# Kernel optimization log

Hardware: AMD Instinct MI355X
Metric: run time of the kernel (lower is better)

## Reference

```python
import jax, jax.numpy as jnp
import numpy as np

VOCAB = 1000
MAX_T = 1000  # max_episode_length
L = 64        # instruction length


def _uniform(key, shape, fan_in, fan_out):
    bound = float(np.sqrt(6.0 / (fan_in + fan_out)))
    return jax.random.uniform(key, shape, jnp.float32, -bound, bound)


def setup_inputs() -> dict:
    key = jax.random.key(0)
    ks = jax.random.split(key, 20)
    s = float(1.0 / np.sqrt(256.0))
    inp = {}
    inp['x'] = jax.random.normal(ks[0], (1, 400), jnp.float32)
    inp['input_inst'] = jax.random.randint(ks[1], (1, L), 0, VOCAB)
    inp['tx'] = jax.random.randint(ks[2], (1,), 0, MAX_T + 1)
    inp['hx'] = jax.random.normal(ks[3], (1, 256), jnp.float32) * 0.1
    inp['cx'] = jax.random.normal(ks[4], (1, 256), jnp.float32) * 0.1
    inp['img1_w'] = _uniform(ks[5], (128, 400), 400, 128); inp['img1_b'] = jnp.zeros((128,), jnp.float32)
    inp['img2_w'] = _uniform(ks[6], (128, 128), 128, 128); inp['img2_b'] = jnp.zeros((128,), jnp.float32)
    inp['img3_w'] = _uniform(ks[7], (128, 128), 128, 128); inp['img3_b'] = jnp.zeros((128,), jnp.float32)
    inp['emb'] = jax.random.normal(ks[8], (VOCAB, 32), jnp.float32)
    inp['gru_wi'] = jax.random.uniform(ks[9], (768, 32), jnp.float32, -s, s)
    inp['gru_wh'] = jax.random.uniform(ks[10], (768, 256), jnp.float32, -s, s)
    inp['gru_bi'] = jnp.zeros((768,), jnp.float32); inp['gru_bh'] = jnp.zeros((768,), jnp.float32)
    inp['attn_w'] = _uniform(ks[11], (128, 256), 256, 128); inp['attn_b'] = jnp.zeros((128,), jnp.float32)
    inp['time_emb'] = jax.random.normal(ks[12], (MAX_T + 1, 32), jnp.float32)
    inp['lin_w'] = _uniform(ks[13], (256, 128), 128, 256); inp['lin_b'] = jnp.zeros((256,), jnp.float32)
    inp['lstm_wi'] = jax.random.uniform(ks[14], (1024, 256), jnp.float32, -s, s)
    inp['lstm_wh'] = jax.random.uniform(ks[15], (1024, 256), jnp.float32, -s, s)
    inp['lstm_bi'] = jnp.zeros((1024,), jnp.float32); inp['lstm_bh'] = jnp.zeros((1024,), jnp.float32)
    inp['crit_w'] = jax.random.normal(ks[16], (1, 288), jnp.float32) * 0.06
    inp['crit_b'] = jnp.zeros((1,), jnp.float32)
    inp['act_w'] = jax.random.normal(ks[17], (4, 288), jnp.float32) * 0.01
    inp['act_b'] = jnp.zeros((4,), jnp.float32)
    return inp


def _linear(x, w, b):
    return x @ w.T + b


def reference(x, input_inst, tx, hx, cx,
              img1_w, img1_b, img2_w, img2_b, img3_w, img3_b,
              emb, gru_wi, gru_wh, gru_bi, gru_bh,
              attn_w, attn_b, time_emb, lin_w, lin_b,
              lstm_wi, lstm_wh, lstm_bi, lstm_bh,
              crit_w, crit_b, act_w, act_b):
    # image MLP: 400 -> 128 -> 128 -> 128
    h = jax.nn.relu(_linear(x.reshape(x.shape[0], -1), img1_w, img1_b))
    h = jax.nn.relu(_linear(h, img2_w, img2_b))
    x_image_rep = jax.nn.relu(_linear(h, img3_w, img3_b))  # (1,128)

    # GRU encoder over instruction tokens (torch gate order: r, z, n)
    emb_seq = emb[input_inst[0]]  # (L, 32)

    def gru_step(hg, e):
        gi = gru_wi @ e + gru_bi        # (768,)
        gh = gru_wh @ hg + gru_bh       # (768,)
        ir, iz, i_n = jnp.split(gi, 3)
        hr, hz, hn = jnp.split(gh, 3)
        r = jax.nn.sigmoid(ir + hr)
        z = jax.nn.sigmoid(iz + hz)
        n = jnp.tanh(i_n + r * hn)
        return (1.0 - z) * n + z * hg, None

    h_enc, _ = jax.lax.scan(gru_step, jnp.zeros((256,), x.dtype), emb_seq)
    x_instr_rep = h_enc[None, :]  # (1,256)

    # gated attention fusion
    x_attention = jax.nn.sigmoid(_linear(x_instr_rep, attn_w, attn_b))  # (1,128)
    fused = x_image_rep * x_attention
    fused = jax.nn.relu(_linear(fused, lin_w, lin_b))  # (1,256)

    # LSTMCell (torch gate order: i, f, g, o)
    gates = fused @ lstm_wi.T + lstm_bi + hx @ lstm_wh.T + lstm_bh  # (1,1024)
    i_g, f_g, g_g, o_g = jnp.split(gates, 4, axis=1)
    c_new = jax.nn.sigmoid(f_g) * cx + jax.nn.sigmoid(i_g) * jnp.tanh(g_g)
    h_new = jax.nn.sigmoid(o_g) * jnp.tanh(c_new)

    t_emb = time_emb[tx].reshape(-1, 32)  # (1,32)
    feat = jnp.concatenate([h_new, t_emb], axis=1)  # (1,288)
    return _linear(feat, crit_w, crit_b), _linear(feat, act_w, act_b), h_new, c_new
```

## Files before the change

### kernel.cpp

```cpp
#include <hip/hip_runtime.h>
#include <math.h>


#define SENT_U 0xFFC0DEADu

#define WS_HBUF   0
#define WS_FLAGS  16640
#define WS_IMG    16704
#define WS_GATESH 16832
#define WS_FUSED  17856
#define WS_HNEW   18112

__device__ __forceinline__ float dot4(const float4 a, const float4 b){
  return a.x*b.x + a.y*b.y + a.z*b.z + a.w*b.w;
}
__device__ __forceinline__ float sigm(float x){ return 1.f/(1.f+expf(-x)); }
__device__ __forceinline__ float aload(const float* p){
  return __hip_atomic_load(p, __ATOMIC_RELAXED, __HIP_MEMORY_SCOPE_AGENT);
}
__device__ __forceinline__ void astore(float* p, float v){
  __hip_atomic_store(p, v, __ATOMIC_RELAXED, __HIP_MEMORY_SCOPE_AGENT);
}

__global__ __launch_bounds__(256) void a3c_init(float* __restrict__ ws){
  const int i = blockIdx.x*256 + threadIdx.x;
  ((unsigned*)(ws + WS_HBUF + 256))[i] = SENT_U;
  if (i < 2) ((int*)(ws + WS_FLAGS))[i] = 0;
}

__global__ __launch_bounds__(256) void a3c_main(
    const int*   __restrict__ inst, const float* __restrict__ emb,
    const float* __restrict__ gwi,  const float* __restrict__ gwh,
    const float* __restrict__ gbi,  const float* __restrict__ gbh,
    const float* __restrict__ x,
    const float* __restrict__ i1w,  const float* __restrict__ i1b,
    const float* __restrict__ i2w,  const float* __restrict__ i2b,
    const float* __restrict__ i3w,  const float* __restrict__ i3b,
    const float* __restrict__ hx,   const float* __restrict__ lwh,
    const float* __restrict__ lbh,  float* __restrict__ ws)
{
  const int b = blockIdx.x;
  const int t = threadIdx.x;

  if (b < 8) {
    __shared__ __align__(16) float h_lds[256];
    __shared__ float gi_lds[64*96];
    __shared__ __align__(16) float emb_lds[64*32];
    const int u   = t >> 3;
    const int sub = t & 7;
    const int U   = b*32 + u;

    float4 wv0[8], wv1[8], wv2[8];
    {
      const float4* p0 = (const float4*)(gwh + (0*256 + U)*256 + sub*32);
      const float4* p1 = (const float4*)(gwh + (1*256 + U)*256 + sub*32);
      const float4* p2 = (const float4*)(gwh + (2*256 + U)*256 + sub*32);
      #pragma unroll
      for (int k=0;k<8;++k){ wv0[k]=p0[k]; wv1[k]=p1[k]; wv2[k]=p2[k]; }
    }
    const float bh0 = gbh[U], bh1 = gbh[256+U], bh2 = gbh[512+U];

    for (int i=t; i<64*32; i+=256)
      emb_lds[i] = emb[inst[i>>5]*32 + (i&31)];
    h_lds[t] = 0.f;
    __syncthreads();

    if (t < 192){
      const int lr = t>>1, half = t&1;
      const int g = lr>>5, ul = lr&31;
      const int grow = (g<<8) + b*32 + ul;
      float4 wi[8];
      const float4* wip = (const float4*)(gwi + grow*32);
      #pragma unroll
      for (int k=0;k<8;++k) wi[k]=wip[k];
      const float bi = gbi[grow];
      for (int s=half*32; s<half*32+32; ++s){
        const float4* e4 = (const float4*)(emb_lds + s*32);
        float acc = bi;
        #pragma unroll
        for (int k=0;k<8;++k) acc += dot4(wi[k], e4[k]);
        gi_lds[s*96 + lr] = acc;
      }
    }
    __syncthreads();

    float* hb = ws + WS_HBUF;
    for (int s=0; s<64; ++s){
      const float4* h4 = (const float4*)(h_lds + sub*32);
      float p0=0.f, p1=0.f, p2=0.f;
      #pragma unroll
      for (int k=0;k<8;++k){
        const float4 h = h4[k];
        p0 += dot4(wv0[k], h);
        p1 += dot4(wv1[k], h);
        p2 += dot4(wv2[k], h);
      }
      #pragma unroll
      for (int off=4; off; off>>=1){
        p0 += __shfl_down(p0, off, 8);
        p1 += __shfl_down(p1, off, 8);
        p2 += __shfl_down(p2, off, 8);
      }
      const float h_old = h_lds[U];
      if (sub == 0){
        const float* gis = gi_lds + s*96;
        const float r = sigm(gis[u]      + p0 + bh0);
        const float z = sigm(gis[32 + u] + p1 + bh1);
        const float n = tanhf(gis[64 + u] + r*(p2 + bh2));
        astore(&hb[(s+1)*256 + U], (1.f - z)*n + z*h_old);
      }
      __syncthreads();
      float v;
      do { v = aload(&hb[(s+1)*256 + t]); } while (__float_as_uint(v) == SENT_U);
      h_lds[t] = v;
      __syncthreads();
    }

  } else if (b == 8) {
    __shared__ __align__(16) float x_lds[400];
    __shared__ __align__(16) float h1[128];
    __shared__ __align__(16) float h2[128];
    x_lds[t] = x[t];
    if (t < 144) x_lds[256+t] = x[256+t];
    __syncthreads();
    {
      const int o = t>>1, half = t&1;
      const float4* wr = (const float4*)(i1w + o*400 + half*200);
      const float4* xr = (const float4*)(x_lds + half*200);
      float acc = 0.f;
      #pragma unroll 5
      for (int k=0;k<50;++k) acc += dot4(wr[k], xr[k]);
      acc += __shfl_down(acc, 1, 2);
      if (half == 0) h1[o] = fmaxf(acc + i1b[o], 0.f);
    }
    __syncthreads();
    if (t < 128){
      const float4* wr = (const float4*)(i2w + t*128);
      const float4* h4 = (const float4*)h1;
      float acc = i2b[t];
      #pragma unroll 8
      for (int k=0;k<32;++k) acc += dot4(wr[k], h4[k]);
      h2[t] = fmaxf(acc, 0.f);
    }
    __syncthreads();
    if (t < 128){
      const float4* wr = (const float4*)(i3w + t*128);
      const float4* h4 = (const float4*)h2;
      float acc = i3b[t];
      #pragma unroll 8
      for (int k=0;k<32;++k) acc += dot4(wr[k], h4[k]);
      ws[WS_IMG + t] = fmaxf(acc, 0.f);
    }

  } else {
    __shared__ __align__(16) float hx_lds[256];
    hx_lds[t] = hx[t];
    __syncthreads();
    const int R = (b-9)*256 + t;
    const float4* wr = (const float4*)(lwh + R*256);
    const float4* h4 = (const float4*)hx_lds;
    float acc = lbh[R];
    #pragma unroll 8
    for (int k=0;k<64;++k) acc += dot4(wr[k], h4[k]);
    ws[WS_GATESH + R] = acc;
  }
}

__global__ __launch_bounds__(256) void a3c_tail(
    const float* __restrict__ aw,  const float* __restrict__ ab,
    const float* __restrict__ lw,  const float* __restrict__ lb,
    const float* __restrict__ lwi, const float* __restrict__ lbi,
    const float* __restrict__ cx,  const int*   __restrict__ tx,
    const float* __restrict__ temb,
    const float* __restrict__ cw,  const float* __restrict__ cb,
    const float* __restrict__ acw, const float* __restrict__ acb,
    float* __restrict__ ws, float* __restrict__ out)
{
  const int b = blockIdx.x;
  const int t = threadIdx.x;
  int* F = (int*)(ws + WS_FLAGS);

  if (b == 0) {
    __shared__ __align__(16) float henc[256];
    __shared__ __align__(16) float f0[128];
    __shared__ __align__(16) float feat[288];
    __shared__ float red[4];
    henc[t] = ws[WS_HBUF + 64*256 + t];
    __syncthreads();
    if (t < 128){
      const float4* wr = (const float4*)(aw + t*256);
      const float4* h4 = (const float4*)henc;
      float acc = ab[t];
      #pragma unroll 8
      for (int k=0;k<64;++k) acc += dot4(wr[k], h4[k]);
      f0[t] = ws[WS_IMG + t] * sigm(acc);
    }
    __syncthreads();
    {
      const float4* wr = (const float4*)(lw + t*128);
      const float4* h4 = (const float4*)f0;
      float acc = lb[t];
      #pragma unroll 8
      for (int k=0;k<32;++k) acc += dot4(wr[k], h4[k]);
      astore(ws + WS_FUSED + t, fmaxf(acc, 0.f));
    }
    __syncthreads();
    if (t == 0){
      __threadfence();
      __hip_atomic_store(&F[0], 1, __ATOMIC_RELEASE, __HIP_MEMORY_SCOPE_AGENT);
      while (__hip_atomic_load(&F[1], __ATOMIC_ACQUIRE, __HIP_MEMORY_SCOPE_AGENT) < 4){}
    }
    __syncthreads();
    feat[t] = aload(ws + WS_HNEW + t);
    if (t < 32) feat[256+t] = temb[tx[0]*32 + t];
    __syncthreads();
    for (int o=0; o<5; ++o){
      const float* wrow = (o==0) ? cw : (acw + (o-1)*288);
      float pr = feat[t]*wrow[t];
      if (t < 32) pr += feat[256+t]*wrow[256+t];
      #pragma unroll
      for (int off=32; off; off>>=1) pr += __shfl_down(pr, off, 64);
      if ((t&63)==0) red[t>>6] = pr;
      __syncthreads();
      if (t == 0) out[o] = red[0]+red[1]+red[2]+red[3] + (o==0 ? cb[0] : acb[o-1]);
      __syncthreads();
    }

  } else {
    const int p = b - 1;
    __shared__ __align__(16) float fused_lds[256];
    __shared__ float gv[256];
    const int g = t >> 6, ul = t & 63;
    const int R = (g<<8) + p*64 + ul;
    const float4* wr = (const float4*)(lwi + R*256);
    float pf = 0.f;
    for (int k=0;k<64;++k){ float4 w = wr[k]; pf += w.x+w.y+w.z+w.w; }
    asm volatile("" :: "v"(pf));
    const float gh = ws[WS_GATESH + R] + lbi[R];
    if (t == 0){
      while (__hip_atomic_load(&F[0], __ATOMIC_ACQUIRE, __HIP_MEMORY_SCOPE_AGENT) == 0){}
    }
    __syncthreads();
    fused_lds[t] = aload(ws + WS_FUSED + t);
    __syncthreads();
    float acc = gh;
    const float4* f4 = (const float4*)fused_lds;
    #pragma unroll 8
    for (int k=0;k<64;++k) acc += dot4(wr[k], f4[k]);
    gv[t] = acc;
    __syncthreads();
    if (t < 64){
      const int u2 = p*64 + t;
      const float iv = gv[t], fv = gv[64+t], gg = gv[128+t], ov = gv[192+t];
      const float c = sigm(fv)*cx[u2] + sigm(iv)*tanhf(gg);
      const float h = sigm(ov)*tanhf(c);
      out[5   + u2] = h;
      out[261 + u2] = c;
      astore(ws + WS_HNEW + u2, h);
    }
    __syncthreads();
    if (t == 0){
      __threadfence();
      __hip_atomic_fetch_add(&F[1], 1, __ATOMIC_RELEASE, __HIP_MEMORY_SCOPE_AGENT);
    }
  }
}

extern "C" void kernel_launch(void* const* d_in, const int* in_sizes, int n_in,
                              void* d_out, int out_size, void* d_ws, size_t ws_size,
                              hipStream_t stream) {
  (void)in_sizes; (void)n_in; (void)out_size; (void)ws_size;
  const float* x    = (const float*)d_in[0];
  const int*   inst = (const int*)  d_in[1];
  const int*   tx   = (const int*)  d_in[2];
  const float* hx   = (const float*)d_in[3];
  const float* cx   = (const float*)d_in[4];
  const float* i1w  = (const float*)d_in[5];
  const float* i1b  = (const float*)d_in[6];
  const float* i2w  = (const float*)d_in[7];
  const float* i2b  = (const float*)d_in[8];
  const float* i3w  = (const float*)d_in[9];
  const float* i3b  = (const float*)d_in[10];
  const float* emb  = (const float*)d_in[11];
  const float* gwi  = (const float*)d_in[12];
  const float* gwh  = (const float*)d_in[13];
  const float* gbi  = (const float*)d_in[14];
  const float* gbh  = (const float*)d_in[15];
  const float* aw   = (const float*)d_in[16];
  const float* ab   = (const float*)d_in[17];
  const float* temb = (const float*)d_in[18];
  const float* lw   = (const float*)d_in[19];
  const float* lb   = (const float*)d_in[20];
  const float* lwi  = (const float*)d_in[21];
  const float* lwh  = (const float*)d_in[22];
  const float* lbi  = (const float*)d_in[23];
  const float* lbh  = (const float*)d_in[24];
  const float* cw   = (const float*)d_in[25];
  const float* cb   = (const float*)d_in[26];
  const float* acw  = (const float*)d_in[27];
  const float* acb  = (const float*)d_in[28];
  float* ws  = (float*)d_ws;
  float* out = (float*)d_out;

  a3c_init<<<64, 256, 0, stream>>>(ws);
  a3c_main<<<13, 256, 0, stream>>>(inst, emb, gwi, gwh, gbi, gbh,
                                   x, i1w, i1b, i2w, i2b, i3w, i3b,
                                   hx, lwh, lbh, ws);
  a3c_tail<<<5, 256, 0, stream>>>(aw, ab, lw, lb, lwi, lbi, cx, tx, temb,
                                  cw, cb, acw, acb, ws, out);
}
```

Baseline: 151.2 us.

## Run GRU scan in one 768-thread block with fp16 register-resident weights

Replaces the 8-block GRU recurrence, which synchronised through global-memory sentinel polling, with a single 768-thread workgroup. Each thread keeps one full row of the hidden-weight matrix as packed fp16 in registers and uses fdot2, so each step needs only LDS and __syncthreads. Kernels are reordered into pre/scan/post and the flag spin-waits are dropped. Output heads are now summed with atomicAdd. The costs are reduced fp16 precision, heavy register pressure (128 packed regs per thread) and one workgroup doing all the serial work.

New measurement: 174.4 us. 15.4% more time.

```diff
diff --git a/kernel.cpp b/kernel.cpp
--- a/kernel.cpp
+++ b/kernel.cpp
@@ -2,124 +2,36 @@
 #include <math.h>
 
 
-#define SENT_U 0xFFC0DEADu
-
-#define WS_HBUF   0
-#define WS_FLAGS  16640
-#define WS_IMG    16704
-#define WS_GATESH 16832
-#define WS_FUSED  17856
-#define WS_HNEW   18112
+typedef __fp16 h2 __attribute__((ext_vector_type(2)));
+
+#define WS_IMG    0
+#define WS_GATESH 128
+#define WS_FUSED  1152
 
 __device__ __forceinline__ float dot4(const float4 a, const float4 b){
   return a.x*b.x + a.y*b.y + a.z*b.z + a.w*b.w;
 }
 __device__ __forceinline__ float sigm(float x){ return 1.f/(1.f+expf(-x)); }
-__device__ __forceinline__ float aload(const float* p){
-  return __hip_atomic_load(p, __ATOMIC_RELAXED, __HIP_MEMORY_SCOPE_AGENT);
-}
-__device__ __forceinline__ void astore(float* p, float v){
-  __hip_atomic_store(p, v, __ATOMIC_RELAXED, __HIP_MEMORY_SCOPE_AGENT);
-}
-
-__global__ __launch_bounds__(256) void a3c_init(float* __restrict__ ws){
-  const int i = blockIdx.x*256 + threadIdx.x;
-  ((unsigned*)(ws + WS_HBUF + 256))[i] = SENT_U;
-  if (i < 2) ((int*)(ws + WS_FLAGS))[i] = 0;
-}
-
-__global__ __launch_bounds__(256) void a3c_main(
-    const int*   __restrict__ inst, const float* __restrict__ emb,
-    const float* __restrict__ gwi,  const float* __restrict__ gwh,
-    const float* __restrict__ gbi,  const float* __restrict__ gbh,
+
+__global__ __launch_bounds__(256) void a3c_pre(
     const float* __restrict__ x,
-    const float* __restrict__ i1w,  const float* __restrict__ i1b,
-    const float* __restrict__ i2w,  const float* __restrict__ i2b,
-    const float* __restrict__ i3w,  const float* __restrict__ i3b,
-    const float* __restrict__ hx,   const float* __restrict__ lwh,
-    const float* __restrict__ lbh,  float* __restrict__ ws)
+    const float* __restrict__ i1w, const float* __restrict__ i1b,
+    const float* __restrict__ i2w, const float* __restrict__ i2b,
+    const float* __restrict__ i3w, const float* __restrict__ i3b,
+    const float* __restrict__ hx,  const float* __restrict__ lwh,
+    const float* __restrict__ lbh,
+    const int*   __restrict__ tx,  const float* __restrict__ temb,
+    const float* __restrict__ cw,  const float* __restrict__ cb,
+    const float* __restrict__ acw, const float* __restrict__ acb,
+    float* __restrict__ ws, float* __restrict__ out)
 {
   const int b = blockIdx.x;
   const int t = threadIdx.x;
 
-  if (b < 8) {
-    __shared__ __align__(16) float h_lds[256];
-    __shared__ float gi_lds[64*96];
-    __shared__ __align__(16) float emb_lds[64*32];
-    const int u   = t >> 3;
-    const int sub = t & 7;
-    const int U   = b*32 + u;
-
-    float4 wv0[8], wv1[8], wv2[8];
-    {
-      const float4* p0 = (const float4*)(gwh + (0*256 + U)*256 + sub*32);
-      const float4* p1 = (const float4*)(gwh + (1*256 + U)*256 + sub*32);
-      const float4* p2 = (const float4*)(gwh + (2*256 + U)*256 + sub*32);
-      #pragma unroll
-      for (int k=0;k<8;++k){ wv0[k]=p0[k]; wv1[k]=p1[k]; wv2[k]=p2[k]; }
-    }
-    const float bh0 = gbh[U], bh1 = gbh[256+U], bh2 = gbh[512+U];
-
-    for (int i=t; i<64*32; i+=256)
-      emb_lds[i] = emb[inst[i>>5]*32 + (i&31)];
-    h_lds[t] = 0.f;
-    __syncthreads();
-
-    if (t < 192){
-      const int lr = t>>1, half = t&1;
-      const int g = lr>>5, ul = lr&31;
-      const int grow = (g<<8) + b*32 + ul;
-      float4 wi[8];
-      const float4* wip = (const float4*)(gwi + grow*32);
-      #pragma unroll
-      for (int k=0;k<8;++k) wi[k]=wip[k];
-      const float bi = gbi[grow];
-      for (int s=half*32; s<half*32+32; ++s){
-        const float4* e4 = (const float4*)(emb_lds + s*32);
-        float acc = bi;
-        #pragma unroll
-        for (int k=0;k<8;++k) acc += dot4(wi[k], e4[k]);
-        gi_lds[s*96 + lr] = acc;
-      }
-    }
-    __syncthreads();
-
-    float* hb = ws + WS_HBUF;
-    for (int s=0; s<64; ++s){
-      const float4* h4 = (const float4*)(h_lds + sub*32);
-      float p0=0.f, p1=0.f, p2=0.f;
-      #pragma unroll
-      for (int k=0;k<8;++k){
-        const float4 h = h4[k];
-        p0 += dot4(wv0[k], h);
-        p1 += dot4(wv1[k], h);
-        p2 += dot4(wv2[k], h);
-      }
-      #pragma unroll
-      for (int off=4; off; off>>=1){
-        p0 += __shfl_down(p0, off, 8);
-        p1 += __shfl_down(p1, off, 8);
-        p2 += __shfl_down(p2, off, 8);
-      }
-      const float h_old = h_lds[U];
-      if (sub == 0){
-        const float* gis = gi_lds + s*96;
-        const float r = sigm(gis[u]      + p0 + bh0);
-        const float z = sigm(gis[32 + u] + p1 + bh1);
-        const float n = tanhf(gis[64 + u] + r*(p2 + bh2));
-        astore(&hb[(s+1)*256 + U], (1.f - z)*n + z*h_old);
-      }
-      __syncthreads();
-      float v;
-      do { v = aload(&hb[(s+1)*256 + t]); } while (__float_as_uint(v) == SENT_U);
-      h_lds[t] = v;
-      __syncthreads();
-    }
-
-  } else if (b == 8) {
+  if (b == 0) {
     __shared__ __align__(16) float x_lds[400];
     __shared__ __align__(16) float h1[128];
-    __shared__ __align__(16) float h2[128];
+    __shared__ __align__(16) float h2s[128];
     x_lds[t] = x[t];
     if (t < 144) x_lds[256+t] = x[256+t];
     __syncthreads();
@@ -140,23 +52,37 @@
       float acc = i2b[t];
       #pragma unroll 8
       for (int k=0;k<32;++k) acc += dot4(wr[k], h4[k]);
-      h2[t] = fmaxf(acc, 0.f);
+      h2s[t] = fmaxf(acc, 0.f);
     }
     __syncthreads();
     if (t < 128){
       const float4* wr = (const float4*)(i3w + t*128);
-      const float4* h4 = (const float4*)h2;
+      const float4* h4 = (const float4*)h2s;
       float acc = i3b[t];
       #pragma unroll 8
       for (int k=0;k<32;++k) acc += dot4(wr[k], h4[k]);
       ws[WS_IMG + t] = fmaxf(acc, 0.f);
     }
 
+  } else if (b == 5) {
+    if (t < 64){
+      float tv = 0.f;
+      if (t < 32) tv = temb[tx[0]*32 + t];
+      #pragma unroll
+      for (int o=0;o<5;++o){
+        const float* wrow = (o==0) ? cw : (acw + (o-1)*288);
+        float pr = (t < 32) ? tv*wrow[256+t] : 0.f;
+        #pragma unroll
+        for (int off=16; off; off>>=1) pr += __shfl_down(pr, off, 32);
+        if (t == 0) out[o] = pr + ((o==0) ? cb[0] : acb[o-1]);
+      }
+    }
+
   } else {
     __shared__ __align__(16) float hx_lds[256];
     hx_lds[t] = hx[t];
     __syncthreads();
-    const int R = (b-9)*256 + t;
+    const int R = (b-1)*256 + t;
     const float4* wr = (const float4*)(lwh + R*256);
     const float4* h4 = (const float4*)hx_lds;
     float acc = lbh[R];
@@ -166,102 +92,147 @@
   }
 }
 
-__global__ __launch_bounds__(256) void a3c_tail(
-    const float* __restrict__ aw,  const float* __restrict__ ab,
-    const float* __restrict__ lw,  const float* __restrict__ lb,
+__global__ __launch_bounds__(768) void a3c_scan(
+    const int*   __restrict__ inst, const float* __restrict__ emb,
+    const float* __restrict__ gwi,  const float* __restrict__ gwh,
+    const float* __restrict__ gbi,  const float* __restrict__ gbh,
+    const float* __restrict__ aw,   const float* __restrict__ ab,
+    const float* __restrict__ lw,   const float* __restrict__ lb,
+    float* __restrict__ ws)
+{
+  const int t = threadIdx.x;
+  __shared__ __fp16 gi16[64*768];
+  __shared__ __align__(16) h2 e16[1024];
+  __shared__ __align__(16) float h32[256];
+  __shared__ __align__(16) h2 h16[128];
+  __shared__ float pre[768];
+  __shared__ float hn[256];
+  __shared__ __align__(16) float f0[128];
+
+  for (int i=t; i<2048; i+=768)
+    ((__fp16*)e16)[i] = (__fp16)emb[inst[i>>5]*32 + (i&31)];
+  const float bh_t = gbh[t];
+  const float bi_t = gbi[t];
+  __syncthreads();
+
+  {
+    h2 wi[16];
+    const float4* wp = (const float4*)(gwi + t*32);
+    #pragma unroll
+    for (int k=0;k<8;++k){
+      float4 w = wp[k];
+      wi[2*k]   = __builtin_amdgcn_cvt_pkrtz(w.x, w.y);
+      wi[2*k+1] = __builtin_amdgcn_cvt_pkrtz(w.z, w.w);
+    }
+    for (int s=0;s<64;++s){
+      const h2* ep = e16 + s*16;
+      float a0 = bi_t, a1 = 0.f;
+      #pragma unroll
+      for (int k=0;k<8;++k)  a0 = __builtin_amdgcn_fdot2(wi[k], ep[k], a0, false);
+      #pragma unroll
+      for (int k=8;k<16;++k) a1 = __builtin_amdgcn_fdot2(wi[k], ep[k], a1, false);
+      gi16[s*768 + t] = (__fp16)(a0 + a1);
+    }
+  }
+
+  h2 wh[128];
+  {
+    const float4* wp = (const float4*)(gwh + t*256);
+    #pragma unroll
+    for (int k=0;k<64;++k){
+      float4 w = wp[k];
+      wh[2*k]   = __builtin_amdgcn_cvt_pkrtz(w.x, w.y);
+      wh[2*k+1] = __builtin_amdgcn_cvt_pkrtz(w.z, w.w);
+    }
+  }
+  if (t < 256){ h32[t] = 0.f; ((__fp16*)h16)[t] = (__fp16)0.f; }
+  __syncthreads();
+
+  for (int s=0;s<64;++s){
+    const float gi_s = (float)gi16[s*768 + t];
+    float a0 = bh_t, a1 = 0.f, a2 = 0.f, a3 = 0.f;
+    #pragma unroll
+    for (int k=0;  k<32; ++k) a0 = __builtin_amdgcn_fdot2(wh[k], h16[k], a0, false);
+    #pragma unroll
+    for (int k=32; k<64; ++k) a1 = __builtin_amdgcn_fdot2(wh[k], h16[k], a1, false);
+    #pragma unroll
+    for (int k=64; k<96; ++k) a2 = __builtin_amdgcn_fdot2(wh[k], h16[k], a2, false);
+    #pragma unroll
+    for (int k=96; k<128;++k) a3 = __builtin_amdgcn_fdot2(wh[k], h16[k], a3, false);
+    const float acc = (a0+a1)+(a2+a3);
+    if (t < 512) pre[t] = gi_s + acc;
+    else       { pre[t] = gi_s; hn[t-512] = acc; }
+    __syncthreads();
+    if (t < 256){
+      const float r  = sigm(pre[t]);
+      const float z  = sigm(pre[256+t]);
+      const float n  = tanhf(pre[512+t] + r*hn[t]);
+      const float hv = (1.f - z)*n + z*h32[t];
+      h32[t] = hv;
+      ((__fp16*)h16)[t] = (__fp16)hv;
+    }
+    __syncthreads();
+  }
+
+  if (t < 128){
+    const float4* wr = (const float4*)(aw + t*256);
+    const float4* h4 = (const float4*)h32;
+    float acc = ab[t];
+    #pragma unroll 8
+    for (int k=0;k<64;++k) acc += dot4(wr[k], h4[k]);
+    f0[t] = ws[WS_IMG + t] * sigm(acc);
+  }
+  __syncthreads();
+  if (t < 256){
+    const float4* wr = (const float4*)(lw + t*128);
+    const float4* h4 = (const float4*)f0;
+    float acc = lb[t];
+    #pragma unroll 8
+    for (int k=0;k<32;++k) acc += dot4(wr[k], h4[k]);
+    ws[WS_FUSED + t] = fmaxf(acc, 0.f);
+  }
+}
+
+__global__ __launch_bounds__(256) void a3c_post(
     const float* __restrict__ lwi, const float* __restrict__ lbi,
-    const float* __restrict__ cx,  const int*   __restrict__ tx,
-    const float* __restrict__ temb,
-    const float* __restrict__ cw,  const float* __restrict__ cb,
-    const float* __restrict__ acw, const float* __restrict__ acb,
+    const float* __restrict__ cx,
+    const float* __restrict__ cw,  const float* __restrict__ acw,
     float* __restrict__ ws, float* __restrict__ out)
 {
-  const int b = blockIdx.x;
+  const int p = blockIdx.x;
   const int t = threadIdx.x;
-  int* F = (int*)(ws + WS_FLAGS);
-
-  if (b == 0) {
-    __shared__ __align__(16) float henc[256];
-    __shared__ __align__(16) float f0[128];
-    __shared__ __align__(16) float feat[288];
-    __shared__ float red[4];
-    henc[t] = ws[WS_HBUF + 64*256 + t];
-    __syncthreads();
-    if (t < 128){
-      const float4* wr = (const float4*)(aw + t*256);
-      const float4* h4 = (const float4*)henc;
-      float acc = ab[t];
-      #pragma unroll 8
-      for (int k=0;k<64;++k) acc += dot4(wr[k], h4[k]);
-      f0[t] = ws[WS_IMG + t] * sigm(acc);
-    }
-    __syncthreads();
-    {
-      const float4* wr = (const float4*)(lw + t*128);
-      const float4* h4 = (const float4*)f0;
-      float acc = lb[t];
-      #pragma unroll 8
-      for (int k=0;k<32;++k) acc += dot4(wr[k], h4[k]);
-      astore(ws + WS_FUSED + t, fmaxf(acc, 0.f));
-    }
-    __syncthreads();
-    if (t == 0){
-      __threadfence();
-      __hip_atomic_store(&F[0], 1, __ATOMIC_RELEASE, __HIP_MEMORY_SCOPE_AGENT);
-      while (__hip_atomic_load(&F[1], __ATOMIC_ACQUIRE, __HIP_MEMORY_SCOPE_AGENT) < 4){}
-    }
-    __syncthreads();
-    feat[t] = aload(ws + WS_HNEW + t);
-    if (t < 32) feat[256+t] = temb[tx[0]*32 + t];
-    __syncthreads();
-    for (int o=0; o<5; ++o){
+  __shared__ __align__(16) float fused_lds[256];
+  __shared__ float gv[256];
+  __shared__ float hh[64];
+  fused_lds[t] = ws[WS_FUSED + t];
+  __syncthreads();
+  const int g = t>>6, ul = t&63;
+  const int R = (g<<8) + p*64 + ul;
+  const float4* wr = (const float4*)(lwi + R*256);
+  const float4* f4 = (const float4*)fused_lds;
+  float acc = ws[WS_GATESH + R] + lbi[R];
+  #pragma unroll 8
+  for (int k=0;k<64;++k) acc += dot4(wr[k], f4[k]);
+  gv[t] = acc;
+  __syncthreads();
+  if (t < 64){
+    const int u2 = p*64 + t;
+    const float iv = gv[t], fv = gv[64+t], gg = gv[128+t], ov = gv[192+t];
+    const float c = sigm(fv)*cx[u2] + sigm(iv)*tanhf(gg);
+    const float h = sigm(ov)*tanhf(c);
+    out[5   + u2] = h;
+    out[261 + u2] = c;
+    hh[t] = h;
+  }
+  __syncthreads();
+  if (t < 64){
+    #pragma unroll
+    for (int o=0;o<5;++o){
       const float* wrow = (o==0) ? cw : (acw + (o-1)*288);
-      float pr = feat[t]*wrow[t];
-      if (t < 32) pr += feat[256+t]*wrow[256+t];
+      float pr = hh[t]*wrow[p*64 + t];
       #pragma unroll
       for (int off=32; off; off>>=1) pr += __shfl_down(pr, off, 64);
-      if ((t&63)==0) red[t>>6] = pr;
-      __syncthreads();
-      if (t == 0) out[o] = red[0]+red[1]+red[2]+red[3] + (o==0 ? cb[0] : acb[o-1]);
-      __syncthreads();
-    }
-
-  } else {
-    const int p = b - 1;
-    __shared__ __align__(16) float fused_lds[256];
-    __shared__ float gv[256];
-    const int g = t >> 6, ul = t & 63;
-    const int R = (g<<8) + p*64 + ul;
-    const float4* wr = (const float4*)(lwi + R*256);
-    float pf = 0.f;
-    for (int k=0;k<64;++k){ float4 w = wr[k]; pf += w.x+w.y+w.z+w.w; }
-    asm volatile("" :: "v"(pf));
-    const float gh = ws[WS_GATESH + R] + lbi[R];
-    if (t == 0){
-      while (__hip_atomic_load(&F[0], __ATOMIC_ACQUIRE, __HIP_MEMORY_SCOPE_AGENT) == 0){}
-    }
-    __syncthreads();
-    fused_lds[t] = aload(ws + WS_FUSED + t);
-    __syncthreads();
-    float acc = gh;
-    const float4* f4 = (const float4*)fused_lds;
-    #pragma unroll 8
-    for (int k=0;k<64;++k) acc += dot4(wr[k], f4[k]);
-    gv[t] = acc;
-    __syncthreads();
-    if (t < 64){
-      const int u2 = p*64 + t;
-      const float iv = gv[t], fv = gv[64+t], gg = gv[128+t], ov = gv[192+t];
-      const float c = sigm(fv)*cx[u2] + sigm(iv)*tanhf(gg);
-      const float h = sigm(ov)*tanhf(c);
-      out[5   + u2] = h;
-      out[261 + u2] = c;
-      astore(ws + WS_HNEW + u2, h);
-    }
-    __syncthreads();
-    if (t == 0){
-      __threadfence();
-      __hip_atomic_fetch_add(&F[1], 1, __ATOMIC_RELEASE, __HIP_MEMORY_SCOPE_AGENT);
+      if (t == 0) atomicAdd(out + o, pr);
     }
   }
 }
@@ -302,10 +273,10 @@
   float* ws  = (float*)d_ws;
   float* out = (float*)d_out;
 
-  a3c_init<<<64, 256, 0, stream>>>(ws);
-  a3c_main<<<13, 256, 0, stream>>>(inst, emb, gwi, gwh, gbi, gbh,
-                                   x, i1w, i1b, i2w, i2b, i3w, i3b,
-                                   hx, lwh, lbh, ws);
-  a3c_tail<<<5, 256, 0, stream>>>(aw, ab, lw, lb, lwi, lbi, cx, tx, temb,
-                                  cw, cb, acw, acb, ws, out);
-}
+  a3c_pre <<<6, 256, 0, stream>>>(x, i1w, i1b, i2w, i2b, i3w, i3b,
+                                  hx, lwh, lbh, tx, temb, cw, cb, acw, acb,
+                                  ws, out);
+  a3c_scan<<<1, 768, 0, stream>>>(inst, emb, gwi, gwh, gbi, gbh,
+                                  aw, ab, lw, lb, ws);
+  a3c_post<<<4, 256, 0, stream>>>(lwi, lbi, cx, cw, acw, ws, out);
+}
```

## Co-locate GRU scan blocks on one XCD and restructure tail into post kernel

Applied to the files above, without the earlier changes.

Launches 120 candidate blocks and reads the XCC id from a hardware register, so that the first XCD to gather eight arrivals supplies the eight GRU-scan blocks. The 64-step per-step spin exchange then stays within one L2 and avoids cross-die coherence latency. The attention and fusion stage moves into scan block 0, which spin-waits on a sentinel-initialised image buffer. The LSTM and output heads move into a separate 4-block kernel that accumulates head outputs with atomicAdd, replacing the inter-block flag handshake. This adds launch overhead from surplus blocks and relies on the undocumented register layout and on co-residency for progress.

Result: faster. 147.6 us (-2.4%).

```diff
diff --git a/kernel.cpp b/kernel.cpp
--- a/kernel.cpp
+++ b/kernel.cpp
@@ -5,11 +5,12 @@
 #define SENT_U 0xFFC0DEADu
 
 #define WS_HBUF   0
-#define WS_FLAGS  16640
-#define WS_IMG    16704
-#define WS_GATESH 16832
-#define WS_FUSED  17856
-#define WS_HNEW   18112
+#define WS_CNT    16640
+#define WS_DESIG  16656
+#define WS_WTK    16657
+#define WS_IMG    16660
+#define WS_GATESH 16788
+#define WS_FUSED  17812
 
 __device__ __forceinline__ float dot4(const float4 a, const float4 b){
   return a.x*b.x + a.y*b.y + a.z*b.z + a.w*b.w;
@@ -23,177 +24,216 @@
 }
 
 __global__ __launch_bounds__(256) void a3c_init(float* __restrict__ ws){
-  const int i = blockIdx.x*256 + threadIdx.x;
-  ((unsigned*)(ws + WS_HBUF + 256))[i] = SENT_U;
-  if (i < 2) ((int*)(ws + WS_FLAGS))[i] = 0;
-}
-
-__global__ __launch_bounds__(256) void a3c_main(
+  const int b = blockIdx.x, t = threadIdx.x;
+  if (b < 64){
+    ((unsigned*)(ws + WS_HBUF + 256))[b*256 + t] = SENT_U;
+  } else {
+    if (t < 128)               ((unsigned*)(ws + WS_IMG))[t] = SENT_U;
+    else if (t < 144)          ((int*)(ws + WS_CNT))[t-128] = 0;
+    else if (t == 144)         ((int*)(ws + WS_DESIG))[0] = -1;
+    else if (t == 145)         ((int*)(ws + WS_WTK))[0] = 0;
+  }
+}
+
+__global__ __launch_bounds__(256) void a3c_scan(
     const int*   __restrict__ inst, const float* __restrict__ emb,
     const float* __restrict__ gwi,  const float* __restrict__ gwh,
     const float* __restrict__ gbi,  const float* __restrict__ gbh,
+    const float* __restrict__ aw,   const float* __restrict__ ab,
+    const float* __restrict__ lw,   const float* __restrict__ lb,
     const float* __restrict__ x,
     const float* __restrict__ i1w,  const float* __restrict__ i1b,
     const float* __restrict__ i2w,  const float* __restrict__ i2b,
     const float* __restrict__ i3w,  const float* __restrict__ i3b,
     const float* __restrict__ hx,   const float* __restrict__ lwh,
-    const float* __restrict__ lbh,  float* __restrict__ ws)
-{
-  const int b = blockIdx.x;
-  const int t = threadIdx.x;
-
-  if (b < 8) {
-    __shared__ __align__(16) float h_lds[256];
-    __shared__ float gi_lds[64*96];
-    __shared__ __align__(16) float emb_lds[64*32];
-    const int u   = t >> 3;
-    const int sub = t & 7;
-    const int U   = b*32 + u;
-
-    float4 wv0[8], wv1[8], wv2[8];
-    {
-      const float4* p0 = (const float4*)(gwh + (0*256 + U)*256 + sub*32);
-      const float4* p1 = (const float4*)(gwh + (1*256 + U)*256 + sub*32);
-      const float4* p2 = (const float4*)(gwh + (2*256 + U)*256 + sub*32);
-      #pragma unroll
-      for (int k=0;k<8;++k){ wv0[k]=p0[k]; wv1[k]=p1[k]; wv2[k]=p2[k]; }
-    }
-    const float bh0 = gbh[U], bh1 = gbh[256+U], bh2 = gbh[512+U];
-
-    for (int i=t; i<64*32; i+=256)
-      emb_lds[i] = emb[inst[i>>5]*32 + (i&31)];
-    h_lds[t] = 0.f;
-    __syncthreads();
-
-    if (t < 192){
-      const int lr = t>>1, half = t&1;
-      const int g = lr>>5, ul = lr&31;
-      const int grow = (g<<8) + b*32 + ul;
-      float4 wi[8];
-      const float4* wip = (const float4*)(gwi + grow*32);
-      #pragma unroll
-      for (int k=0;k<8;++k) wi[k]=wip[k];
-      const float bi = gbi[grow];
-      for (int s=half*32; s<half*32+32; ++s){
-        const float4* e4 = (const float4*)(emb_lds + s*32);
-        float acc = bi;
-        #pragma unroll
-        for (int k=0;k<8;++k) acc += dot4(wi[k], e4[k]);
-        gi_lds[s*96 + lr] = acc;
-      }
-    }
-    __syncthreads();
-
-    float* hb = ws + WS_HBUF;
-    for (int s=0; s<64; ++s){
-      const float4* h4 = (const float4*)(h_lds + sub*32);
-      float p0=0.f, p1=0.f, p2=0.f;
-      #pragma unroll
-      for (int k=0;k<8;++k){
-        const float4 h = h4[k];
-        p0 += dot4(wv0[k], h);
-        p1 += dot4(wv1[k], h);
-        p2 += dot4(wv2[k], h);
-      }
-      #pragma unroll
-      for (int off=4; off; off>>=1){
-        p0 += __shfl_down(p0, off, 8);
-        p1 += __shfl_down(p1, off, 8);
-        p2 += __shfl_down(p2, off, 8);
-      }
-      const float h_old = h_lds[U];
-      if (sub == 0){
-        const float* gis = gi_lds + s*96;
-        const float r = sigm(gis[u]      + p0 + bh0);
-        const float z = sigm(gis[32 + u] + p1 + bh1);
-        const float n = tanhf(gis[64 + u] + r*(p2 + bh2));
-        astore(&hb[(s+1)*256 + U], (1.f - z)*n + z*h_old);
-      }
-      __syncthreads();
-      float v;
-      do { v = aload(&hb[(s+1)*256 + t]); } while (__float_as_uint(v) == SENT_U);
-      h_lds[t] = v;
-      __syncthreads();
-    }
-
-  } else if (b == 8) {
-    __shared__ __align__(16) float x_lds[400];
-    __shared__ __align__(16) float h1[128];
-    __shared__ __align__(16) float h2[128];
-    x_lds[t] = x[t];
-    if (t < 144) x_lds[256+t] = x[256+t];
-    __syncthreads();
-    {
-      const int o = t>>1, half = t&1;
-      const float4* wr = (const float4*)(i1w + o*400 + half*200);
-      const float4* xr = (const float4*)(x_lds + half*200);
-      float acc = 0.f;
-      #pragma unroll 5
-      for (int k=0;k<50;++k) acc += dot4(wr[k], xr[k]);
-      acc += __shfl_down(acc, 1, 2);
-      if (half == 0) h1[o] = fmaxf(acc + i1b[o], 0.f);
-    }
-    __syncthreads();
-    if (t < 128){
-      const float4* wr = (const float4*)(i2w + t*128);
-      const float4* h4 = (const float4*)h1;
-      float acc = i2b[t];
-      #pragma unroll 8
-      for (int k=0;k<32;++k) acc += dot4(wr[k], h4[k]);
-      h2[t] = fmaxf(acc, 0.f);
-    }
-    __syncthreads();
-    if (t < 128){
-      const float4* wr = (const float4*)(i3w + t*128);
-      const float4* h4 = (const float4*)h2;
-      float acc = i3b[t];
-      #pragma unroll 8
-      for (int k=0;k<32;++k) acc += dot4(wr[k], h4[k]);
-      ws[WS_IMG + t] = fmaxf(acc, 0.f);
-    }
-
-  } else {
-    __shared__ __align__(16) float hx_lds[256];
-    hx_lds[t] = hx[t];
-    __syncthreads();
-    const int R = (b-9)*256 + t;
-    const float4* wr = (const float4*)(lwh + R*256);
-    const float4* h4 = (const float4*)hx_lds;
-    float acc = lbh[R];
-    #pragma unroll 8
-    for (int k=0;k<64;++k) acc += dot4(wr[k], h4[k]);
-    ws[WS_GATESH + R] = acc;
-  }
-}
-
-__global__ __launch_bounds__(256) void a3c_tail(
-    const float* __restrict__ aw,  const float* __restrict__ ab,
-    const float* __restrict__ lw,  const float* __restrict__ lb,
-    const float* __restrict__ lwi, const float* __restrict__ lbi,
-    const float* __restrict__ cx,  const int*   __restrict__ tx,
-    const float* __restrict__ temb,
-    const float* __restrict__ cw,  const float* __restrict__ cb,
-    const float* __restrict__ acw, const float* __restrict__ acb,
+    const float* __restrict__ lbh,
+    const int*   __restrict__ tx,   const float* __restrict__ temb,
+    const float* __restrict__ cw,   const float* __restrict__ cb,
+    const float* __restrict__ acw,  const float* __restrict__ acb,
     float* __restrict__ ws, float* __restrict__ out)
 {
   const int b = blockIdx.x;
   const int t = threadIdx.x;
-  int* F = (int*)(ws + WS_FLAGS);
-
-  if (b == 0) {
-    __shared__ __align__(16) float henc[256];
-    __shared__ __align__(16) float f0[128];
-    __shared__ __align__(16) float feat[288];
-    __shared__ float red[4];
-    henc[t] = ws[WS_HBUF + 64*256 + t];
+
+  if (b >= 120){
+    if (b == 120){
+      __shared__ __align__(16) float x_lds[400];
+      __shared__ __align__(16) float h1[128];
+      __shared__ __align__(16) float h2s[128];
+      x_lds[t] = x[t];
+      if (t < 144) x_lds[256+t] = x[256+t];
+      __syncthreads();
+      {
+        const int o = t>>1, half = t&1;
+        const float4* wr = (const float4*)(i1w + o*400 + half*200);
+        const float4* xr = (const float4*)(x_lds + half*200);
+        float acc = 0.f;
+        #pragma unroll 5
+        for (int k=0;k<50;++k) acc += dot4(wr[k], xr[k]);
+        acc += __shfl_down(acc, 1, 2);
+        if (half == 0) h1[o] = fmaxf(acc + i1b[o], 0.f);
+      }
+      __syncthreads();
+      if (t < 128){
+        const float4* wr = (const float4*)(i2w + t*128);
+        const float4* h4 = (const float4*)h1;
+        float acc = i2b[t];
+        #pragma unroll 8
+        for (int k=0;k<32;++k) acc += dot4(wr[k], h4[k]);
+        h2s[t] = fmaxf(acc, 0.f);
+      }
+      __syncthreads();
+      if (t < 128){
+        const float4* wr = (const float4*)(i3w + t*128);
+        const float4* h4 = (const float4*)h2s;
+        float acc = i3b[t];
+        #pragma unroll 8
+        for (int k=0;k<32;++k) acc += dot4(wr[k], h4[k]);
+        astore(ws + WS_IMG + t, fmaxf(acc, 0.f));
+      }
+    } else if (b == 125){
+      if (t < 64){
+        float tv = 0.f;
+        if (t < 32) tv = temb[tx[0]*32 + t];
+        #pragma unroll
+        for (int o=0;o<5;++o){
+          const float* wrow = (o==0) ? cw : (acw + (o-1)*288);
+          float pr = (t < 32) ? tv*wrow[256+t] : 0.f;
+          #pragma unroll
+          for (int off=16; off; off>>=1) pr += __shfl_down(pr, off, 32);
+          if (t == 0) out[o] = pr + ((o==0) ? cb[0] : acb[o-1]);
+        }
+      }
+    } else {
+      __shared__ __align__(16) float hx_lds[256];
+      hx_lds[t] = hx[t];
+      __syncthreads();
+      const int R = (b-121)*256 + t;
+      const float4* wr = (const float4*)(lwh + R*256);
+      const float4* h4 = (const float4*)hx_lds;
+      float acc = lbh[R];
+      #pragma unroll 8
+      for (int k=0;k<64;++k) acc += dot4(wr[k], h4[k]);
+      ws[WS_GATESH + R] = acc;
+    }
+    return;
+  }
+
+  __shared__ int s_role;
+  if (t == 0){
+    unsigned xcc;
+    asm volatile("s_getreg_b32 %0, hwreg(20, 0, 4)" : "=s"(xcc));
+    xcc &= 7u;
+    int* cnt   = (int*)(ws + WS_CNT);
+    int* desig = (int*)(ws + WS_DESIG);
+    int* wtk   = (int*)(ws + WS_WTK);
+    const int arr = __hip_atomic_fetch_add(&cnt[xcc], 1, __ATOMIC_RELAXED,
+                                           __HIP_MEMORY_SCOPE_AGENT);
+    if (arr == 7){
+      int exp = -1;
+      __hip_atomic_compare_exchange_strong(desig, &exp, (int)xcc,
+          __ATOMIC_RELEASE, __ATOMIC_RELAXED, __HIP_MEMORY_SCOPE_AGENT);
+    }
+    int d;
+    while ((d = __hip_atomic_load(desig, __ATOMIC_ACQUIRE,
+                                  __HIP_MEMORY_SCOPE_AGENT)) < 0)
+      __builtin_amdgcn_s_sleep(2);
+    int role = -1;
+    if ((int)xcc == d){
+      const int tk = __hip_atomic_fetch_add(wtk, 1, __ATOMIC_RELAXED,
+                                            __HIP_MEMORY_SCOPE_AGENT);
+      if (tk < 8) role = tk;
+    }
+    s_role = role;
+  }
+  __syncthreads();
+  const int r = s_role;
+  if (r < 0) return;
+
+  __shared__ __align__(16) float h_lds[256];
+  __shared__ float gi_lds[64*96];
+  __shared__ __align__(16) float emb_lds[64*32];
+  __shared__ __align__(16) float f0[128];
+  const int u   = t >> 3;
+  const int sub = t & 7;
+  const int U   = r*32 + u;
+
+  float4 wv0[8], wv1[8], wv2[8];
+  {
+    const float4* p0 = (const float4*)(gwh + (0*256 + U)*256 + sub*32);
+    const float4* p1 = (const float4*)(gwh + (1*256 + U)*256 + sub*32);
+    const float4* p2 = (const float4*)(gwh + (2*256 + U)*256 + sub*32);
+    #pragma unroll
+    for (int k=0;k<8;++k){ wv0[k]=p0[k]; wv1[k]=p1[k]; wv2[k]=p2[k]; }
+  }
+  const float bh0 = gbh[U], bh1 = gbh[256+U], bh2 = gbh[512+U];
+
+  for (int i=t; i<64*32; i+=256)
+    emb_lds[i] = emb[inst[i>>5]*32 + (i&31)];
+  h_lds[t] = 0.f;
+  __syncthreads();
+
+  if (t < 192){
+    const int lr = t>>1, half = t&1;
+    const int g = lr>>5, ul = lr&31;
+    const int grow = (g<<8) + r*32 + ul;
+    float4 wi[8];
+    const float4* wip = (const float4*)(gwi + grow*32);
+    #pragma unroll
+    for (int k=0;k<8;++k) wi[k]=wip[k];
+    const float bi = gbi[grow];
+    for (int s=half*32; s<half*32+32; ++s){
+      const float4* e4 = (const float4*)(emb_lds + s*32);
+      float acc = bi;
+      #pragma unroll
+      for (int k=0;k<8;++k) acc += dot4(wi[k], e4[k]);
+      gi_lds[s*96 + lr] = acc;
+    }
+  }
+  __syncthreads();
+
+  float* hb = ws + WS_HBUF;
+  for (int s=0; s<64; ++s){
+    const float4* h4 = (const float4*)(h_lds + sub*32);
+    float p0=0.f, p1=0.f, p2=0.f;
+    #pragma unroll
+    for (int k=0;k<8;++k){
+      const float4 h = h4[k];
+      p0 += dot4(wv0[k], h);
+      p1 += dot4(wv1[k], h);
+      p2 += dot4(wv2[k], h);
+    }
+    #pragma unroll
+    for (int off=4; off; off>>=1){
+      p0 += __shfl_down(p0, off, 8);
+      p1 += __shfl_down(p1, off, 8);
+      p2 += __shfl_down(p2, off, 8);
+    }
+    const float h_old = h_lds[U];
+    if (sub == 0){
+      const float* gis = gi_lds + s*96;
+      const float rr = sigm(gis[u]      + p0 + bh0);
+      const float zz = sigm(gis[32 + u] + p1 + bh1);
+      const float nn = tanhf(gis[64 + u] + rr*(p2 + bh2));
+      astore(&hb[(s+1)*256 + U], (1.f - zz)*nn + zz*h_old);
+    }
     __syncthreads();
+    float v;
+    do { v = aload(&hb[(s+1)*256 + t]); } while (__float_as_uint(v) == SENT_U);
+    h_lds[t] = v;
+    __syncthreads();
+  }
+
+  if (r == 0){
+    float im = 0.f;
     if (t < 128){
+      do { im = aload(ws + WS_IMG + t); } while (__float_as_uint(im) == SENT_U);
       const float4* wr = (const float4*)(aw + t*256);
-      const float4* h4 = (const float4*)henc;
+      const float4* h4 = (const float4*)h_lds;
       float acc = ab[t];
       #pragma unroll 8
       for (int k=0;k<64;++k) acc += dot4(wr[k], h4[k]);
-      f0[t] = ws[WS_IMG + t] * sigm(acc);
+      f0[t] = im * sigm(acc);
     }
     __syncthreads();
     {
@@ -202,66 +242,51 @@
       float acc = lb[t];
       #pragma unroll 8
       for (int k=0;k<32;++k) acc += dot4(wr[k], h4[k]);
-      astore(ws + WS_FUSED + t, fmaxf(acc, 0.f));
-    }
-    __syncthreads();
-    if (t == 0){
-      __threadfence();
-      __hip_atomic_store(&F[0], 1, __ATOMIC_RELEASE, __HIP_MEMORY_SCOPE_AGENT);
-      while (__hip_atomic_load(&F[1], __ATOMIC_ACQUIRE, __HIP_MEMORY_SCOPE_AGENT) < 4){}
-    }
-    __syncthreads();
-    feat[t] = aload(ws + WS_HNEW + t);
-    if (t < 32) feat[256+t] = temb[tx[0]*32 + t];
-    __syncthreads();
-    for (int o=0; o<5; ++o){
+      ws[WS_FUSED + t] = fmaxf(acc, 0.f);
+    }
+  }
+}
+
+__global__ __launch_bounds__(256) void a3c_post(
+    const float* __restrict__ lwi, const float* __restrict__ lbi,
+    const float* __restrict__ cx,
+    const float* __restrict__ cw,  const float* __restrict__ acw,
+    float* __restrict__ ws, float* __restrict__ out)
+{
+  const int p = blockIdx.x;
+  const int t = threadIdx.x;
+  __shared__ __align__(16) float fused_lds[256];
+  __shared__ float gv[256];
+  __shared__ float hh[64];
+  fused_lds[t] = ws[WS_FUSED + t];
+  __syncthreads();
+  const int g = t>>6, ul = t&63;
+  const int R = (g<<8) + p*64 + ul;
+  const float4* wr = (const float4*)(lwi + R*256);
+  const float4* f4 = (const float4*)fused_lds;
+  float acc = ws[WS_GATESH + R] + lbi[R];
+  #pragma unroll 8
+  for (int k=0;k<64;++k) acc += dot4(wr[k], f4[k]);
+  gv[t] = acc;
+  __syncthreads();
+  if (t < 64){
+    const int u2 = p*64 + t;
+    const float iv = gv[t], fv = gv[64+t], gg = gv[128+t], ov = gv[192+t];
+    const float c = sigm(fv)*cx[u2] + sigm(iv)*tanhf(gg);
+    const float h = sigm(ov)*tanhf(c);
+    out[5   + u2] = h;
+    out[261 + u2] = c;
+    hh[t] = h;
+  }
+  __syncthreads();
+  if (t < 64){
+    #pragma unroll
+    for (int o=0;o<5;++o){
       const float* wrow = (o==0) ? cw : (acw + (o-1)*288);
-      float pr = feat[t]*wrow[t];
-      if (t < 32) pr += feat[256+t]*wrow[256+t];
+      float pr = hh[t]*wrow[p*64 + t];
       #pragma unroll
       for (int off=32; off; off>>=1) pr += __shfl_down(pr, off, 64);
-      if ((t&63)==0) red[t>>6] = pr;
-      __syncthreads();
-      if (t == 0) out[o] = red[0]+red[1]+red[2]+red[3] + (o==0 ? cb[0] : acb[o-1]);
-      __syncthreads();
-    }
-
-  } else {
-    const int p = b - 1;
-    __shared__ __align__(16) float fused_lds[256];
-    __shared__ float gv[256];
-    const int g = t >> 6, ul = t & 63;
-    const int R = (g<<8) + p*64 + ul;
-    const float4* wr = (const float4*)(lwi + R*256);
-    float pf = 0.f;
-    for (int k=0;k<64;++k){ float4 w = wr[k]; pf += w.x+w.y+w.z+w.w; }
-    asm volatile("" :: "v"(pf));
-    const float gh = ws[WS_GATESH + R] + lbi[R];
-    if (t == 0){
-      while (__hip_atomic_load(&F[0], __ATOMIC_ACQUIRE, __HIP_MEMORY_SCOPE_AGENT) == 0){}
-    }
-    __syncthreads();
-    fused_lds[t] = aload(ws + WS_FUSED + t);
-    __syncthreads();
-    float acc = gh;
-    const float4* f4 = (const float4*)fused_lds;
-    #pragma unroll 8
-    for (int k=0;k<64;++k) acc += dot4(wr[k], f4[k]);
-    gv[t] = acc;
-    __syncthreads();
-    if (t < 64){
-      const int u2 = p*64 + t;
-      const float iv = gv[t], fv = gv[64+t], gg = gv[128+t], ov = gv[192+t];
-      const float c = sigm(fv)*cx[u2] + sigm(iv)*tanhf(gg);
-      const float h = sigm(ov)*tanhf(c);
-      out[5   + u2] = h;
-      out[261 + u2] = c;
-      astore(ws + WS_HNEW + u2, h);
-    }
-    __syncthreads();
-    if (t == 0){
-      __threadfence();
-      __hip_atomic_fetch_add(&F[1], 1, __ATOMIC_RELEASE, __HIP_MEMORY_SCOPE_AGENT);
+      if (t == 0) atomicAdd(out + o, pr);
     }
   }
 }
@@ -302,10 +327,11 @@
   float* ws  = (float*)d_ws;
   float* out = (float*)d_out;
 
-  a3c_init<<<64, 256, 0, stream>>>(ws);
-  a3c_main<<<13, 256, 0, stream>>>(inst, emb, gwi, gwh, gbi, gbh,
-                                   x, i1w, i1b, i2w, i2b, i3w, i3b,
-                                   hx, lwh, lbh, ws);
-  a3c_tail<<<5, 256, 0, stream>>>(aw, ab, lw, lb, lwi, lbi, cx, tx, temb,
-                                  cw, cb, acw, acb, ws, out);
-}
+  a3c_init<<<65, 256, 0, stream>>>(ws);
+  a3c_scan<<<126, 256, 0, stream>>>(inst, emb, gwi, gwh, gbi, gbh,
+                                    aw, ab, lw, lb,
+                                    x, i1w, i1b, i2w, i2b, i3w, i3b,
+                                    hx, lwh, lbh, tx, temb, cw, cb, acw, acb,
+                                    ws, out);
+  a3c_post<<<4, 256, 0, stream>>>(lwi, lbi, cx, cw, acw, ws, out);
+}
```
